# Kernel optimization log

Measured on AMD Instinct MI355X. Metric: run time of the kernel, lower is better.

The kernel has to match this reference:

```python
import jax, jax.numpy as jnp
import numpy as np

EMB_BOUND = 0.000316
T, E, D = 16, 100000, 128
B = 4096
L = 20  # fixed bag length used to build offsets (TBE supports ragged; math identical)


def setup_inputs() -> dict:
    key = jax.random.key(0)
    kw, ki = jax.random.split(key)
    weights = jax.random.uniform(kw, (T, E, D), dtype=jnp.float32,
                                 minval=-EMB_BOUND, maxval=EMB_BOUND)
    indices = jax.random.randint(ki, (T * B * L,), 0, E, dtype=jnp.int64)
    offsets = (jnp.arange(T * B + 1, dtype=jnp.int64) * L)
    return {"weights": weights, "indices": indices, "offsets": offsets}


def reference(weights, indices, offsets):
    # weights: [T, E, D]; indices: [N] flat; offsets: [T*B+1], table-major bags.
    n = indices.shape[0]
    num_bags = offsets.shape[0] - 1  # T*B
    b = num_bags // T
    # bag (segment) id for each lookup index
    seg = jnp.searchsorted(offsets, jnp.arange(n, dtype=offsets.dtype), side='right') - 1
    table = seg // b  # which table each lookup belongs to
    flat_w = weights.reshape(T * E, D)
    rows = flat_w[table * E + indices]  # [N, D] irregular gather
    pooled = jax.ops.segment_sum(rows, seg, num_segments=num_bags)  # [T*B, D]
    # table-major -> [B, T*D]
    return pooled.reshape(T, b, D).transpose(1, 0, 2).reshape(b, T * D)
```

## Files before the change

kernel.cpp:

```cpp
#include <hip/hip_runtime.h>


constexpr int T = 16;
constexpr int E = 100000;
constexpr int D = 128;
constexpr int BAGS_PER_TABLE = 4096;
constexpr int NUM_BAGS = T * BAGS_PER_TABLE;
constexpr int WAVES_PER_BLOCK = 4;

__global__ __launch_bounds__(256) void tbe_pool_kernel(
    const float* __restrict__ weights,
    const int* __restrict__ indices,
    const int* __restrict__ offsets,
    float* __restrict__ out)
{
    const int wave = threadIdx.x >> 6;
    const int lane = threadIdx.x & 63;
    const int bag  = blockIdx.x * WAVES_PER_BLOCK + wave;
    if (bag >= NUM_BAGS) return;

    const int t = bag / BAGS_PER_TABLE;
    const int b = bag - t * BAGS_PER_TABLE;

    const int start = offsets[bag];
    const int end   = offsets[bag + 1];

    const float2* __restrict__ tbl =
        reinterpret_cast<const float2*>(weights + (long long)t * E * D);

    float2 a0 = {0.f, 0.f}, a1 = {0.f, 0.f}, a2 = {0.f, 0.f}, a3 = {0.f, 0.f};

    int i = start;
    for (; i + 4 <= end; i += 4) {
        const int i0 = indices[i];
        const int i1 = indices[i + 1];
        const int i2 = indices[i + 2];
        const int i3 = indices[i + 3];
        const float2 v0 = tbl[(long long)i0 * (D / 2) + lane];
        const float2 v1 = tbl[(long long)i1 * (D / 2) + lane];
        const float2 v2 = tbl[(long long)i2 * (D / 2) + lane];
        const float2 v3 = tbl[(long long)i3 * (D / 2) + lane];
        a0.x += v0.x; a0.y += v0.y;
        a1.x += v1.x; a1.y += v1.y;
        a2.x += v2.x; a2.y += v2.y;
        a3.x += v3.x; a3.y += v3.y;
    }
    for (; i < end; ++i) {
        const int i0 = indices[i];
        const float2 v0 = tbl[(long long)i0 * (D / 2) + lane];
        a0.x += v0.x; a0.y += v0.y;
    }

    float2 acc;
    acc.x = (a0.x + a1.x) + (a2.x + a3.x);
    acc.y = (a0.y + a1.y) + (a2.y + a3.y);

    float2* __restrict__ o =
        reinterpret_cast<float2*>(out + (long long)b * (T * D) + t * D);
    o[lane] = acc;
}

extern "C" void kernel_launch(void* const* d_in, const int* in_sizes, int n_in,
                              void* d_out, int out_size, void* d_ws, size_t ws_size,
                              hipStream_t stream) {
    const float* weights = (const float*)d_in[0];
    const int*   indices = (const int*)d_in[1];
    const int*   offsets = (const int*)d_in[2];
    float*       out     = (float*)d_out;

    const int grid = NUM_BAGS / WAVES_PER_BLOCK;
    tbe_pool_kernel<<<grid, 256, 0, stream>>>(weights, indices, offsets, out);
}
```

Baseline: 943.4 us.

## Use float4 loads with two rows per wave and shuffle-broadcast indices

```diff
diff --git a/kernel.cpp b/kernel.cpp
--- a/kernel.cpp
+++ b/kernel.cpp
@@ -4,9 +4,13 @@
 constexpr int T = 16;
 constexpr int E = 100000;
 constexpr int D = 128;
-constexpr int BAGS_PER_TABLE = 4096;
-constexpr int NUM_BAGS = T * BAGS_PER_TABLE;
+constexpr int BPT = 4096;
+constexpr int NUM_BAGS = T * BPT;
 constexpr int WAVES_PER_BLOCK = 4;
+
+__device__ inline void add4(float4& a, const float4& v) {
+    a.x += v.x; a.y += v.y; a.z += v.z; a.w += v.w;
+}
 
 __global__ __launch_bounds__(256) void tbe_pool_kernel(
     const float* __restrict__ weights,
@@ -19,45 +23,89 @@
     const int bag  = blockIdx.x * WAVES_PER_BLOCK + wave;
     if (bag >= NUM_BAGS) return;
 
-    const int t = bag / BAGS_PER_TABLE;
-    const int b = bag - t * BAGS_PER_TABLE;
+    const int t = bag >> 12;
+    const int b = bag & (BPT - 1);
 
     const int start = offsets[bag];
-    const int end   = offsets[bag + 1];
+    const int n     = offsets[bag + 1] - start;
 
-    const float2* __restrict__ tbl =
-        reinterpret_cast<const float2*>(weights + (long long)t * E * D);
+    const int half = lane >> 5;
+    const int col  = lane & 31;
 
-    float2 a0 = {0.f, 0.f}, a1 = {0.f, 0.f}, a2 = {0.f, 0.f}, a3 = {0.f, 0.f};
+    const float4* __restrict__ tbl =
+        reinterpret_cast<const float4*>(weights) + (long long)t * (E * (D / 4));
 
-    int i = start;
-    for (; i + 4 <= end; i += 4) {
-        const int i0 = indices[i];
-        const int i1 = indices[i + 1];
-        const int i2 = indices[i + 2];
-        const int i3 = indices[i + 3];
-        const float2 v0 = tbl[(long long)i0 * (D / 2) + lane];
-        const float2 v1 = tbl[(long long)i1 * (D / 2) + lane];
-        const float2 v2 = tbl[(long long)i2 * (D / 2) + lane];
-        const float2 v3 = tbl[(long long)i3 * (D / 2) + lane];
-        a0.x += v0.x; a0.y += v0.y;
-        a1.x += v1.x; a1.y += v1.y;
-        a2.x += v2.x; a2.y += v2.y;
-        a3.x += v3.x; a3.y += v3.y;
-    }
-    for (; i < end; ++i) {
-        const int i0 = indices[i];
-        const float2 v0 = tbl[(long long)i0 * (D / 2) + lane];
-        a0.x += v0.x; a0.y += v0.y;
+    float4 a0{0,0,0,0}, a1{0,0,0,0}, a2{0,0,0,0}, a3{0,0,0,0};
+
+    if (n <= 64) {
+        int myidx = 0;
+        if (lane < n) myidx = indices[start + lane];
+
+        int j = 0;
+        for (; j + 8 <= n; j += 8) {
+            const int r0 = __shfl(myidx, j + 0 + half);
+            const int r1 = __shfl(myidx, j + 2 + half);
+            const int r2 = __shfl(myidx, j + 4 + half);
+            const int r3 = __shfl(myidx, j + 6 + half);
+            const float4 v0 = tbl[(long long)r0 * (D / 4) + col];
+            const float4 v1 = tbl[(long long)r1 * (D / 4) + col];
+            const float4 v2 = tbl[(long long)r2 * (D / 4) + col];
+            const float4 v3 = tbl[(long long)r3 * (D / 4) + col];
+            add4(a0, v0); add4(a1, v1); add4(a2, v2); add4(a3, v3);
+        }
+        if (j + 4 <= n) {
+            const int r0 = __shfl(myidx, j + 0 + half);
+            const int r1 = __shfl(myidx, j + 2 + half);
+            const float4 v0 = tbl[(long long)r0 * (D / 4) + col];
+            const float4 v1 = tbl[(long long)r1 * (D / 4) + col];
+            add4(a0, v0); add4(a1, v1);
+            j += 4;
+        }
+        if (j + 2 <= n) {
+            const int r0 = __shfl(myidx, j + half);
+            const float4 v0 = tbl[(long long)r0 * (D / 4) + col];
+            add4(a0, v0);
+            j += 2;
+        }
+        if (j < n) {
+            const int r0 = __shfl(myidx, j);
+            if (half == 0) {
+                const float4 v0 = tbl[(long long)r0 * (D / 4) + col];
+                add4(a0, v0);
+            }
+        }
+    } else {
+        int j = 0;
+        for (; j + 2 <= n; j += 2) {
+            const int r = indices[start + j + half];
+            const float4 v = tbl[(long long)r * (D / 4) + col];
+            add4(a0, v);
+        }
+        if (j < n) {
+            const int r = indices[start + j];
+            if (half == 0) {
+                const float4 v = tbl[(long long)r * (D / 4) + col];
+                add4(a0, v);
+            }
+        }
     }
 
-    float2 acc;
+    float4 acc;
     acc.x = (a0.x + a1.x) + (a2.x + a3.x);
     acc.y = (a0.y + a1.y) + (a2.y + a3.y);
+    acc.z = (a0.z + a1.z) + (a2.z + a3.z);
+    acc.w = (a0.w + a1.w) + (a2.w + a3.w);
 
-    float2* __restrict__ o =
-        reinterpret_cast<float2*>(out + (long long)b * (T * D) + t * D);
-    o[lane] = acc;
+    acc.x += __shfl_xor(acc.x, 32);
+    acc.y += __shfl_xor(acc.y, 32);
+    acc.z += __shfl_xor(acc.z, 32);
+    acc.w += __shfl_xor(acc.w, 32);
+
+    if (half == 0) {
+        float4* __restrict__ o =
+            reinterpret_cast<float4*>(out) + (long long)b * (T * D / 4) + t * (D / 4);
+        o[col] = acc;
+    }
 }
 
 extern "C" void kernel_launch(void* const* d_in, const int* in_sizes, int n_in,
```

Result: slower. 971.7 us (+3.0%).
